# Performance work log

Measured on AMD Instinct MI355X. Metric: run time of the kernel, lower is better.

## Reference

```python
import jax, jax.numpy as jnp
import numpy as np

N = 100000
D = 128
E = 1600000
L = 3
LN_EPS = 1e-5
SM_EPS = 1e-16  # PyG softmax denominator eps
NEG_SLOPE = 0.2  # GATConv leaky_relu slope


def setup_inputs() -> dict:
    key = jax.random.key(0)
    ks = jax.random.split(key, 9)
    x = jax.random.normal(ks[0], (N, D), dtype=jnp.float32)
    edge_index = jax.random.randint(ks[1], (2, E), 0, N, dtype=jnp.int64)
    # Per-level GATConv params (heads=1, concat -> out dim D)
    W = jax.random.normal(ks[2], (L, D, D), dtype=jnp.float32) / np.sqrt(D)
    att_src = jax.random.normal(ks[3], (L, D), dtype=jnp.float32) / np.sqrt(D)
    att_dst = jax.random.normal(ks[4], (L, D), dtype=jnp.float32) / np.sqrt(D)
    bias = jnp.zeros((L, D), dtype=jnp.float32)
    ln_gamma = jnp.ones((L, D), dtype=jnp.float32)
    ln_beta = jnp.zeros((L, D), dtype=jnp.float32)
    return {"x": x, "edge_index": edge_index, "W": W, "att_src": att_src,
            "att_dst": att_dst, "bias": bias, "ln_gamma": ln_gamma, "ln_beta": ln_beta}


def _gat_level(x, src, dst, W, a_src, a_dst, b):
    h = x @ W                                   # [N, D] transformed features
    alpha_s = h @ a_src                         # [N] per-node src attention logit
    alpha_d = h @ a_dst                         # [N]
    alpha = alpha_s[src] + alpha_d[dst]         # [E'] edge logits
    alpha = jax.nn.leaky_relu(alpha, NEG_SLOPE)
    amax = jax.ops.segment_max(alpha, dst, num_segments=N)  # self-loops guarantee nonempty segments
    alpha = jnp.exp(alpha - amax[dst])
    denom = jax.ops.segment_sum(alpha, dst, num_segments=N)
    alpha = alpha / (denom[dst] + SM_EPS)       # segment softmax over incoming edges
    msg = h[src] * alpha[:, None]               # [E', D]
    out = jax.ops.segment_sum(msg, dst, num_segments=N)
    return out + b


def reference(x, edge_index, W, att_src, att_dst, bias, ln_gamma, ln_beta):
    loops = jnp.arange(N, dtype=edge_index.dtype)
    src = jnp.concatenate([edge_index[0], loops])  # PyG GATConv adds self-loops
    dst = jnp.concatenate([edge_index[1], loops])
    for i in range(L):
        x_att = _gat_level(x, src, dst, W[i], att_src[i], att_dst[i], bias[i])
        y = x + x_att
        mu = jnp.mean(y, axis=-1, keepdims=True)
        var = jnp.mean(jnp.square(y - mu), axis=-1, keepdims=True)
        y = (y - mu) * jax.lax.rsqrt(var + LN_EPS) * ln_gamma[i] + ln_beta[i]
        x = jax.nn.relu(y)  # dropout is identity in eval mode
    return x
```

## Files before the change

### kernel.cpp

```cpp
#include <hip/hip_runtime.h>
#include <hip/hip_fp16.h>
#include <cstdint>

#define D 128
#define NEG_SLOPE 0.2f
#define LN_EPS 1e-5f
#define SM_EPS 1e-16f


__global__ void hist_dst(const int* __restrict__ dst, int E, int* __restrict__ deg) {
    int e = blockIdx.x * blockDim.x + threadIdx.x;
    if (e < E) atomicAdd(&deg[dst[e]], 1);
}

__global__ void scanA(const int* __restrict__ deg, int n,
                      int* __restrict__ excl, int* __restrict__ bsums) {
    __shared__ int s[256];
    int t = threadIdx.x;
    int v = blockIdx.x * 256 + t;
    int d = (v < n) ? deg[v] : 0;
    s[t] = d;
    __syncthreads();
    for (int off = 1; off < 256; off <<= 1) {
        int tv = (t >= off) ? s[t - off] : 0;
        __syncthreads();
        s[t] += tv;
        __syncthreads();
    }
    if (v < n) excl[v] = s[t] - d;
    if (t == 255) bsums[blockIdx.x] = s[255];
}

__global__ void scanB(int* __restrict__ bsums, int nb) {
    __shared__ int s[512];
    int t = threadIdx.x;
    int v = (t < nb) ? bsums[t] : 0;
    s[t] = v;
    __syncthreads();
    for (int off = 1; off < 512; off <<= 1) {
        int tv = (t >= off) ? s[t - off] : 0;
        __syncthreads();
        s[t] += tv;
        __syncthreads();
    }
    if (t < nb) bsums[t] = s[t] - v;
}

__global__ void scanC(int* __restrict__ rowptr, const int* __restrict__ bsums,
                      int* __restrict__ cursor, int n, int total) {
    int v = blockIdx.x * blockDim.x + threadIdx.x;
    if (v < n) { rowptr[v] += bsums[v >> 8]; cursor[v] = 0; }
    if (v == 0) rowptr[n] = total;
}

__global__ void fill_csr(const int* __restrict__ src, const int* __restrict__ dst,
                         int E, const int* __restrict__ rowptr,
                         int* __restrict__ cursor, int* __restrict__ col) {
    int e = blockIdx.x * blockDim.x + threadIdx.x;
    if (e >= E) return;
    int d = dst[e];
    int p = rowptr[d] + atomicAdd(&cursor[d], 1);
    col[p] = src[e];
}


__global__ __launch_bounds__(256) void gemm_alpha(
        const float* __restrict__ x, const float* __restrict__ W,
        const float* __restrict__ asrc, const float* __restrict__ adst,
        __half* __restrict__ h, float* __restrict__ as_, float* __restrict__ ad_, int n) {
    __shared__ float sX[64][D];
    int t = threadIdx.x;
    int row0 = blockIdx.x * 64;

    const float4* xv = (const float4*)x;
    #pragma unroll
    for (int i = 0; i < 8; ++i) {
        int fid = i * 256 + t;
        int r = fid >> 5;
        int c4 = fid & 31;
        int gr = row0 + r;
        float4 val = (gr < n) ? xv[(size_t)gr * 32 + c4] : make_float4(0.f, 0.f, 0.f, 0.f);
        ((float4*)&sX[r][0])[c4] = val;
    }
    __syncthreads();

    int g = t >> 5, m = t & 31;
    int rbase = g * 8;
    float4 acc[8];
    #pragma unroll
    for (int r = 0; r < 8; ++r) acc[r] = make_float4(0.f, 0.f, 0.f, 0.f);

    const float4* Wv = (const float4*)W;
    #pragma unroll 4
    for (int k = 0; k < D; ++k) {
        float4 w = Wv[k * 32 + m];
        #pragma unroll
        for (int r = 0; r < 8; ++r) {
            float xval = sX[rbase + r][k];
            acc[r].x += xval * w.x;
            acc[r].y += xval * w.y;
            acc[r].z += xval * w.z;
            acc[r].w += xval * w.w;
        }
    }

    float4 a_s = ((const float4*)asrc)[m];
    float4 a_d = ((const float4*)adst)[m];
    #pragma unroll
    for (int r = 0; r < 8; ++r) {
        int gr = row0 + rbase + r;
        if (gr < n) {
            union { __half2 h2[2]; float2 f2; } u;
            u.h2[0] = __floats2half2_rn(acc[r].x, acc[r].y);
            u.h2[1] = __floats2half2_rn(acc[r].z, acc[r].w);
            ((float2*)(h + (size_t)gr * D))[m] = u.f2;
            float ps = acc[r].x * a_s.x + acc[r].y * a_s.y + acc[r].z * a_s.z + acc[r].w * a_s.w;
            float pd = acc[r].x * a_d.x + acc[r].y * a_d.y + acc[r].z * a_d.z + acc[r].w * a_d.w;
            #pragma unroll
            for (int d = 16; d >= 1; d >>= 1) {
                ps += __shfl_xor(ps, d);
                pd += __shfl_xor(pd, d);
            }
            if (m == 0) { as_[gr] = ps; ad_[gr] = pd; }
        }
    }
}


__global__ __launch_bounds__(256) void aggregate(
        const float* __restrict__ xin, const __half* __restrict__ h,
        const float* __restrict__ as_, const float* __restrict__ ad_,
        const int* __restrict__ col, const int* __restrict__ rowptr,
        const float* __restrict__ bias, const float* __restrict__ gamma,
        const float* __restrict__ beta, float* __restrict__ xout, int n) {
    __shared__ int   sS[4][64];
    __shared__ float sA[4][64];
    int tid = threadIdx.x;
    int wslot = tid >> 6;
    int lane = tid & 63;
    int wid = (int)((blockIdx.x * blockDim.x + tid) >> 6);
    if (wid >= n) return;
    int v = wid;
    int grp = lane >> 4;
    int gl  = lane & 15;
    int start = rowptr[v], end = rowptr[v + 1];
    float adv = ad_[v];
    float self_a = as_[v] + adv;
    self_a = (self_a > 0.f) ? self_a : NEG_SLOPE * self_a;

    float mval = self_a;
    for (int cb = start; cb < end; cb += 64) {
        int e = cb + lane;
        int   s_l = 0;
        float a_l = -1e30f;
        if (e < end) {
            s_l = col[e];
            float aa = as_[s_l] + adv;
            a_l = (aa > 0.f) ? aa : NEG_SLOPE * aa;
        }
        if (cb == start) { sS[wslot][lane] = s_l; sA[wslot][lane] = a_l; }
        mval = fmaxf(mval, a_l);
    }
    #pragma unroll
    for (int d = 32; d >= 1; d >>= 1) mval = fmaxf(mval, __shfl_xor(mval, d));

    float sacc = 0.f;
    float acc[8];
    #pragma unroll
    for (int j = 0; j < 8; ++j) acc[j] = 0.f;

    for (int cb = start; cb < end; cb += 64) {
        if (cb != start) {
            int e = cb + lane;
            int   s_l = 0;
            float a_l = -1e30f;
            if (e < end) {
                s_l = col[e];
                float aa = as_[s_l] + adv;
                a_l = (aa > 0.f) ? aa : NEG_SLOPE * aa;
            }
            sS[wslot][lane] = s_l; sA[wslot][lane] = a_l;
        }
        int cnt = min(64, end - cb);
        for (int i = grp; i < cnt; i += 4) {
            int s = sS[wslot][i];
            float w = __expf(sA[wslot][i] - mval);
            sacc += w;
            union { float4 f4; __half2 h2[4]; } u;
            u.f4 = ((const float4*)(h + (size_t)s * D))[gl];
            #pragma unroll
            for (int j = 0; j < 4; ++j) {
                float2 f = __half22float2(u.h2[j]);
                acc[2*j]   += w * f.x;
                acc[2*j+1] += w * f.y;
            }
        }
    }

    sacc += __shfl_xor(sacc, 16);
    sacc += __shfl_xor(sacc, 32);
    #pragma unroll
    for (int j = 0; j < 8; ++j) {
        acc[j] += __shfl_xor(acc[j], 16);
        acc[j] += __shfl_xor(acc[j], 32);
    }

    float w_self = __expf(self_a - mval);
    sacc += w_self;
    {
        union { float4 f4; __half2 h2[4]; } u;
        u.f4 = ((const float4*)(h + (size_t)v * D))[gl];
        #pragma unroll
        for (int j = 0; j < 4; ++j) {
            float2 f = __half22float2(u.h2[j]);
            acc[2*j]   += w_self * f.x;
            acc[2*j+1] += w_self * f.y;
        }
    }
    float inv = 1.f / (sacc + SM_EPS);

    const float4* xr = (const float4*)(xin + (size_t)v * D) + gl * 2;
    float4 xa = xr[0], xb = xr[1];
    const float4* b4 = (const float4*)bias  + gl * 2;
    float4 ba = b4[0], bb = b4[1];
    float y[8];
    y[0] = xa.x + acc[0] * inv + ba.x;
    y[1] = xa.y + acc[1] * inv + ba.y;
    y[2] = xa.z + acc[2] * inv + ba.z;
    y[3] = xa.w + acc[3] * inv + ba.w;
    y[4] = xb.x + acc[4] * inv + bb.x;
    y[5] = xb.y + acc[5] * inv + bb.y;
    y[6] = xb.z + acc[6] * inv + bb.z;
    y[7] = xb.w + acc[7] * inv + bb.w;

    float s2 = 0.f;
    #pragma unroll
    for (int j = 0; j < 8; ++j) s2 += y[j];
    #pragma unroll
    for (int d = 8; d >= 1; d >>= 1) s2 += __shfl_xor(s2, d);
    float mu = s2 * (1.f / 128.f);
    float vs = 0.f;
    #pragma unroll
    for (int j = 0; j < 8; ++j) { float dd = y[j] - mu; vs += dd * dd; }
    #pragma unroll
    for (int d = 8; d >= 1; d >>= 1) vs += __shfl_xor(vs, d);
    float rstd = rsqrtf(vs * (1.f / 128.f) + LN_EPS);

    const float4* g4 = (const float4*)gamma + gl * 2;
    const float4* t4 = (const float4*)beta  + gl * 2;
    float4 ga = g4[0], gb = g4[1];
    float4 ta = t4[0], tb = t4[1];
    float4 oa, ob;
    oa.x = fmaxf((y[0] - mu) * rstd * ga.x + ta.x, 0.f);
    oa.y = fmaxf((y[1] - mu) * rstd * ga.y + ta.y, 0.f);
    oa.z = fmaxf((y[2] - mu) * rstd * ga.z + ta.z, 0.f);
    oa.w = fmaxf((y[3] - mu) * rstd * ga.w + ta.w, 0.f);
    ob.x = fmaxf((y[4] - mu) * rstd * gb.x + tb.x, 0.f);
    ob.y = fmaxf((y[5] - mu) * rstd * gb.y + tb.y, 0.f);
    ob.z = fmaxf((y[6] - mu) * rstd * gb.z + tb.z, 0.f);
    ob.w = fmaxf((y[7] - mu) * rstd * gb.w + tb.w, 0.f);

    if (lane < 16) {
        float4* o4 = (float4*)(xout + (size_t)v * D) + gl * 2;
        o4[0] = oa;
        o4[1] = ob;
    }
}


extern "C" void kernel_launch(void* const* d_in, const int* in_sizes, int n_in,
                              void* d_out, int out_size, void* d_ws, size_t ws_size,
                              hipStream_t stream) {
    const float* x       = (const float*)d_in[0];
    const int*   edge    = (const int*)d_in[1];
    const float* W       = (const float*)d_in[2];
    const float* att_src = (const float*)d_in[3];
    const float* att_dst = (const float*)d_in[4];
    const float* bias    = (const float*)d_in[5];
    const float* gamma   = (const float*)d_in[6];
    const float* beta    = (const float*)d_in[7];
    float* out = (float*)d_out;

    const int N = in_sizes[0] / D;
    const int E = in_sizes[1] / 2;

    const int* src = edge;
    const int* dst = edge + E;

    char* ws = (char*)d_ws;
    size_t off = 0;
    auto carve = [&](size_t bytes) -> char* {
        char* p = ws + off;
        off = (off + bytes + 511) & ~(size_t)511;
        return p;
    };
    int*    rowptr = (int*)carve((size_t)(N + 1) * 4);
    int*    cursor = (int*)carve((size_t)N * 4);
    int*    bsums  = (int*)carve(512 * 4);
    int*    col    = (int*)carve((size_t)E * 4);
    __half* h      = (__half*)carve((size_t)N * D * 2);
    float*  as_    = (float*)carve((size_t)N * 4);
    float*  ad_    = (float*)carve((size_t)N * 4);
    float*  x1     = (float*)carve((size_t)N * D * 4);
    (void)ws_size;

    const int TPB = 256;
    int nbN  = (N + TPB - 1) / TPB;
    int nbE  = (E + TPB - 1) / TPB;

    hipMemsetAsync(cursor, 0, (size_t)N * 4, stream);
    hist_dst<<<nbE, TPB, 0, stream>>>(dst, E, cursor);
    scanA<<<nbN, TPB, 0, stream>>>(cursor, N, rowptr, bsums);
    scanB<<<1, 512, 0, stream>>>(bsums, nbN);
    scanC<<<nbN, TPB, 0, stream>>>(rowptr, bsums, cursor, N, E);
    fill_csr<<<nbE, TPB, 0, stream>>>(src, dst, E, rowptr, cursor, col);

    int gemmGrid = (N + 63) / 64;
    int aggGrid  = (N * 64 + TPB - 1) / TPB;

    const float* xin = x;
    float* bufs[3] = { x1, x1, out };
    for (int l = 0; l < 3; ++l) {
        const float* Wl  = W + (size_t)l * D * D;
        const float* asl = att_src + (size_t)l * D;
        const float* adl = att_dst + (size_t)l * D;
        const float* bl  = bias + (size_t)l * D;
        const float* gl  = gamma + (size_t)l * D;
        const float* btl = beta + (size_t)l * D;
        float* xout = bufs[l];

        gemm_alpha<<<gemmGrid, TPB, 0, stream>>>(xin, Wl, asl, adl, h, as_, ad_, N);
        aggregate<<<aggGrid, TPB, 0, stream>>>(xin, h, as_, ad_, col, rowptr,
                                               bl, gl, btl, xout, N);
        xin = xout;
    }
}
```

Measured before the change: 666.5 us.

## Use MFMA fp16 GEMM with folded attention vectors and half-precision aggregation

Replaces the FP32 scalar GEMM with an fp16 MFMA 16x16x32 kernel over 128-row tiles, staging x and a pre-transposed fp16 W in XOR-swizzled shared memory. A prep kernel folds att_src/att_dst into W (W·a), so the attention logits become dot products of x with precomputed vectors. The aggregation now computes exp weights once per edge instead of per group and accumulates messages with packed half2 FMAs. This cuts GEMM FP32 ALU cost and aggregation arithmetic, at the cost of lower precision: x is rounded to fp16 before the logits are computed, and the weighted sums accumulate in fp16, which risks overflow and accuracy loss.

```diff
diff --git a/kernel.cpp b/kernel.cpp
--- a/kernel.cpp
+++ b/kernel.cpp
@@ -6,6 +6,9 @@
 #define NEG_SLOPE 0.2f
 #define LN_EPS 1e-5f
 #define SM_EPS 1e-16f
+
+typedef _Float16 f16x8 __attribute__((ext_vector_type(8)));
+typedef float f32x4 __attribute__((ext_vector_type(4)));
 
 
 __global__ void hist_dst(const int* __restrict__ dst, int E, int* __restrict__ deg) {
@@ -64,66 +67,131 @@
 }
 
 
-__global__ __launch_bounds__(256) void gemm_alpha(
-        const float* __restrict__ x, const float* __restrict__ W,
-        const float* __restrict__ asrc, const float* __restrict__ adst,
+__global__ void prep_w(const float* __restrict__ W, const float* __restrict__ a_src,
+                       const float* __restrict__ a_dst, __half* __restrict__ Wt,
+                       float* __restrict__ wsv, float* __restrict__ wdv) {
+    int l = blockIdx.x;
+    const float* Wl = W + (size_t)l * D * D;
+    __half* Wtl = Wt + (size_t)l * D * D;
+    int t = threadIdx.x;
+    __shared__ float sA[D], sD[D];
+    if (t < D) { sA[t] = a_src[l * D + t]; sD[t] = a_dst[l * D + t]; }
+    __syncthreads();
+    if (t < D) {
+        float ps = 0.f, pd = 0.f;
+        for (int c = 0; c < D; ++c) {
+            float wv = Wl[t * D + c];
+            ps += wv * sA[c];
+            pd += wv * sD[c];
+        }
+        wsv[l * D + t] = ps;
+        wdv[l * D + t] = pd;
+    }
+    int c = t & 127, kh = t >> 7;
+    for (int g = 0; g < 8; ++g) {
+        int k0 = kh * 64 + g * 8;
+        union { __half hv[8]; float4 f4; } u;
+        #pragma unroll
+        for (int rr = 0; rr < 8; ++rr) u.hv[rr] = __float2half(Wl[(k0 + rr) * D + c]);
+        *(float4*)(Wtl + (size_t)c * D + k0) = u.f4;
+    }
+}
+
+
+__global__ __launch_bounds__(256) void gemm_mfma(
+        const float* __restrict__ x, const __half* __restrict__ Wt,
+        const float* __restrict__ wsv, const float* __restrict__ wdv,
         __half* __restrict__ h, float* __restrict__ as_, float* __restrict__ ad_, int n) {
-    __shared__ float sX[64][D];
+    __shared__ char sXa[32768];
+    __shared__ char sWb[32768];
     int t = threadIdx.x;
-    int row0 = blockIdx.x * 64;
+    int row0 = blockIdx.x * 128;
+    int lane = t & 63;
+    int w = t >> 6;
+    int wrow = (w >> 1) * 64;
+    int wcol = (w & 1) * 64;
 
     const float4* xv = (const float4*)x;
     #pragma unroll
+    for (int i = 0; i < 16; ++i) {
+        int slot = i * 256 + t;
+        int r = slot >> 5;
+        int c4 = slot & 31;
+        int gr = row0 + r;
+        float4 v = (gr < n) ? xv[(size_t)gr * 32 + c4] : make_float4(0.f, 0.f, 0.f, 0.f);
+        union { __half2 q[2]; float2 f; } u;
+        u.q[0] = __floats2half2_rn(v.x, v.y);
+        u.q[1] = __floats2half2_rn(v.z, v.w);
+        *(float2*)(sXa + r * 256 + ((c4 * 8) ^ ((r & 7) << 4))) = u.f;
+    }
+    const float4* wv = (const float4*)Wt;
+    #pragma unroll
     for (int i = 0; i < 8; ++i) {
-        int fid = i * 256 + t;
-        int r = fid >> 5;
-        int c4 = fid & 31;
-        int gr = row0 + r;
-        float4 val = (gr < n) ? xv[(size_t)gr * 32 + c4] : make_float4(0.f, 0.f, 0.f, 0.f);
-        ((float4*)&sX[r][0])[c4] = val;
+        int chunk = i * 256 + t;
+        int r = chunk >> 4;
+        int c16 = chunk & 15;
+        float4 v = wv[chunk];
+        *(float4*)(sWb + r * 256 + ((c16 * 16) ^ ((r & 7) << 4))) = v;
     }
     __syncthreads();
 
-    int g = t >> 5, m = t & 31;
-    int rbase = g * 8;
-    float4 acc[8];
-    #pragma unroll
-    for (int r = 0; r < 8; ++r) acc[r] = make_float4(0.f, 0.f, 0.f, 0.f);
-
-    const float4* Wv = (const float4*)W;
-    #pragma unroll 4
-    for (int k = 0; k < D; ++k) {
-        float4 w = Wv[k * 32 + m];
-        #pragma unroll
-        for (int r = 0; r < 8; ++r) {
-            float xval = sX[rbase + r][k];
-            acc[r].x += xval * w.x;
-            acc[r].y += xval * w.y;
-            acc[r].z += xval * w.z;
-            acc[r].w += xval * w.w;
-        }
-    }
-
-    float4 a_s = ((const float4*)asrc)[m];
-    float4 a_d = ((const float4*)adst)[m];
-    #pragma unroll
-    for (int r = 0; r < 8; ++r) {
-        int gr = row0 + rbase + r;
-        if (gr < n) {
-            union { __half2 h2[2]; float2 f2; } u;
-            u.h2[0] = __floats2half2_rn(acc[r].x, acc[r].y);
-            u.h2[1] = __floats2half2_rn(acc[r].z, acc[r].w);
-            ((float2*)(h + (size_t)gr * D))[m] = u.f2;
-            float ps = acc[r].x * a_s.x + acc[r].y * a_s.y + acc[r].z * a_s.z + acc[r].w * a_s.w;
-            float pd = acc[r].x * a_d.x + acc[r].y * a_d.y + acc[r].z * a_d.z + acc[r].w * a_d.w;
+    f32x4 acc[4][4];
+    #pragma unroll
+    for (int a = 0; a < 4; ++a)
+        #pragma unroll
+        for (int b = 0; b < 4; ++b) acc[a][b] = (f32x4){0.f, 0.f, 0.f, 0.f};
+
+    #pragma unroll
+    for (int ks = 0; ks < 4; ++ks) {
+        int kbyte = ks * 64 + (lane >> 4) * 16;
+        f16x8 aF[4], bF[4];
+        #pragma unroll
+        for (int tt = 0; tt < 4; ++tt) {
+            int ra = wrow + tt * 16 + (lane & 15);
+            aF[tt] = *(f16x8*)(sXa + ra * 256 + (kbyte ^ ((ra & 7) << 4)));
+            int rb = wcol + tt * 16 + (lane & 15);
+            bF[tt] = *(f16x8*)(sWb + rb * 256 + (kbyte ^ ((rb & 7) << 4)));
+        }
+        #pragma unroll
+        for (int tr = 0; tr < 4; ++tr)
             #pragma unroll
-            for (int d = 16; d >= 1; d >>= 1) {
-                ps += __shfl_xor(ps, d);
-                pd += __shfl_xor(pd, d);
+            for (int tc = 0; tc < 4; ++tc)
+                acc[tr][tc] = __builtin_amdgcn_mfma_f32_16x16x32_f16(aF[tr], bF[tc], acc[tr][tc], 0, 0, 0);
+    }
+
+    #pragma unroll
+    for (int tr = 0; tr < 4; ++tr) {
+        #pragma unroll
+        for (int reg = 0; reg < 4; ++reg) {
+            int gr = row0 + wrow + tr * 16 + (lane >> 4) * 4 + reg;
+            if (gr < n) {
+                #pragma unroll
+                for (int tc = 0; tc < 4; ++tc) {
+                    int gc = wcol + tc * 16 + (lane & 15);
+                    h[(size_t)gr * D + gc] = __float2half(acc[tr][tc][reg]);
+                }
             }
-            if (m == 0) { as_[gr] = ps; ad_[gr] = pd; }
-        }
-    }
+        }
+    }
+
+    int r = t >> 1, hh = t & 1;
+    float ps = 0.f, pd = 0.f;
+    const float4* s4 = (const float4*)wsv + hh * 16;
+    const float4* d4 = (const float4*)wdv + hh * 16;
+    #pragma unroll
+    for (int g = 0; g < 8; ++g) {
+        int kbyte = hh * 128 + g * 16;
+        f16x8 xa = *(f16x8*)(sXa + r * 256 + (kbyte ^ ((r & 7) << 4)));
+        float4 sa = s4[g * 2], sb = s4[g * 2 + 1];
+        float4 da = d4[g * 2], db = d4[g * 2 + 1];
+        ps += (float)xa[0] * sa.x + (float)xa[1] * sa.y + (float)xa[2] * sa.z + (float)xa[3] * sa.w
+            + (float)xa[4] * sb.x + (float)xa[5] * sb.y + (float)xa[6] * sb.z + (float)xa[7] * sb.w;
+        pd += (float)xa[0] * da.x + (float)xa[1] * da.y + (float)xa[2] * da.z + (float)xa[3] * da.w
+            + (float)xa[4] * db.x + (float)xa[5] * db.y + (float)xa[6] * db.z + (float)xa[7] * db.w;
+    }
+    ps += __shfl_xor(ps, 1);
+    pd += __shfl_xor(pd, 1);
+    if (hh == 0 && row0 + r < n) { as_[row0 + r] = ps; ad_[row0 + r] = pd; }
 }
 
 
@@ -133,8 +201,8 @@
         const int* __restrict__ col, const int* __restrict__ rowptr,
         const float* __restrict__ bias, const float* __restrict__ gamma,
         const float* __restrict__ beta, float* __restrict__ xout, int n) {
-    __shared__ int   sS[4][64];
-    __shared__ float sA[4][64];
+    __shared__ int     sS[4][64];
+    __shared__ __half2 sW[4][64];
     int tid = threadIdx.x;
     int wslot = tid >> 6;
     int lane = tid & 63;
@@ -149,56 +217,69 @@
     self_a = (self_a > 0.f) ? self_a : NEG_SLOPE * self_a;
 
     float mval = self_a;
+    int   s0 = 0;
+    float a0 = -1e30f;
     for (int cb = start; cb < end; cb += 64) {
         int e = cb + lane;
-        int   s_l = 0;
-        float a_l = -1e30f;
+        int   sl = 0;
+        float al = -1e30f;
         if (e < end) {
-            s_l = col[e];
-            float aa = as_[s_l] + adv;
-            a_l = (aa > 0.f) ? aa : NEG_SLOPE * aa;
-        }
-        if (cb == start) { sS[wslot][lane] = s_l; sA[wslot][lane] = a_l; }
-        mval = fmaxf(mval, a_l);
+            sl = col[e];
+            float aa = as_[sl] + adv;
+            al = (aa > 0.f) ? aa : NEG_SLOPE * aa;
+        }
+        if (cb == start) { s0 = sl; a0 = al; }
+        mval = fmaxf(mval, al);
     }
     #pragma unroll
     for (int d = 32; d >= 1; d >>= 1) mval = fmaxf(mval, __shfl_xor(mval, d));
 
-    float sacc = 0.f;
-    float acc[8];
-    #pragma unroll
-    for (int j = 0; j < 8; ++j) acc[j] = 0.f;
+    float wl = __expf(a0 - mval);
+    float sacc = wl;
+    sS[wslot][lane] = s0;
+    sW[wslot][lane] = __float2half2_rn(wl);
+
+    __half2 hacc[4];
+    #pragma unroll
+    for (int j = 0; j < 4; ++j) hacc[j] = __float2half2_rn(0.f);
+
+    const float4* h4 = (const float4*)h;
 
     for (int cb = start; cb < end; cb += 64) {
         if (cb != start) {
             int e = cb + lane;
-            int   s_l = 0;
-            float a_l = -1e30f;
+            int   sl = 0;
+            float al = -1e30f;
             if (e < end) {
-                s_l = col[e];
-                float aa = as_[s_l] + adv;
-                a_l = (aa > 0.f) ? aa : NEG_SLOPE * aa;
+                sl = col[e];
+                float aa = as_[sl] + adv;
+                al = (aa > 0.f) ? aa : NEG_SLOPE * aa;
             }
-            sS[wslot][lane] = s_l; sA[wslot][lane] = a_l;
+            float wl2 = __expf(al - mval);
+            sacc += wl2;
+            sS[wslot][lane] = sl;
+            sW[wslot][lane] = __float2half2_rn(wl2);
         }
         int cnt = min(64, end - cb);
         for (int i = grp; i < cnt; i += 4) {
             int s = sS[wslot][i];
-            float w = __expf(sA[wslot][i] - mval);
-            sacc += w;
+            __half2 w2 = sW[wslot][i];
             union { float4 f4; __half2 h2[4]; } u;
-            u.f4 = ((const float4*)(h + (size_t)s * D))[gl];
+            u.f4 = h4[(size_t)s * 16 + gl];
             #pragma unroll
-            for (int j = 0; j < 4; ++j) {
-                float2 f = __half22float2(u.h2[j]);
-                acc[2*j]   += w * f.x;
-                acc[2*j+1] += w * f.y;
-            }
-        }
-    }
-
-    sacc += __shfl_xor(sacc, 16);
-    sacc += __shfl_xor(sacc, 32);
+            for (int j = 0; j < 4; ++j) hacc[j] = __hfma2(u.h2[j], w2, hacc[j]);
+        }
+    }
+    #pragma unroll
+    for (int d = 32; d >= 1; d >>= 1) sacc += __shfl_xor(sacc, d);
+
+    float acc[8];
+    #pragma unroll
+    for (int j = 0; j < 4; ++j) {
+        float2 f = __half22float2(hacc[j]);
+        acc[2 * j] = f.x;
+        acc[2 * j + 1] = f.y;
+    }
     #pragma unroll
     for (int j = 0; j < 8; ++j) {
         acc[j] += __shfl_xor(acc[j], 16);
@@ -209,19 +290,19 @@
     sacc += w_self;
     {
         union { float4 f4; __half2 h2[4]; } u;
-        u.f4 = ((const float4*)(h + (size_t)v * D))[gl];
+        u.f4 = h4[(size_t)v * 16 + gl];
         #pragma unroll
         for (int j = 0; j < 4; ++j) {
             float2 f = __half22float2(u.h2[j]);
-            acc[2*j]   += w_self * f.x;
-            acc[2*j+1] += w_self * f.y;
+            acc[2 * j]     += w_self * f.x;
+            acc[2 * j + 1] += w_self * f.y;
         }
     }
     float inv = 1.f / (sacc + SM_EPS);
 
     const float4* xr = (const float4*)(xin + (size_t)v * D) + gl * 2;
     float4 xa = xr[0], xb = xr[1];
-    const float4* b4 = (const float4*)bias  + gl * 2;
+    const float4* b4 = (const float4*)bias + gl * 2;
     float4 ba = b4[0], bb = b4[1];
     float y[8];
     y[0] = xa.x + acc[0] * inv + ba.x;
@@ -247,7 +328,7 @@
     float rstd = rsqrtf(vs * (1.f / 128.f) + LN_EPS);
 
     const float4* g4 = (const float4*)gamma + gl * 2;
-    const float4* t4 = (const float4*)beta  + gl * 2;
+    const float4* t4 = (const float4*)beta + gl * 2;
     float4 ga = g4[0], gb = g4[1];
     float4 ta = t4[0], tb = t4[1];
     float4 oa, ob;
@@ -302,11 +383,16 @@
     float*  as_    = (float*)carve((size_t)N * 4);
     float*  ad_    = (float*)carve((size_t)N * 4);
     float*  x1     = (float*)carve((size_t)N * D * 4);
+    __half* Wt     = (__half*)carve((size_t)3 * D * D * 2);
+    float*  wsv    = (float*)carve((size_t)3 * D * 4);
+    float*  wdv    = (float*)carve((size_t)3 * D * 4);
     (void)ws_size;
 
     const int TPB = 256;
-    int nbN  = (N + TPB - 1) / TPB;
-    int nbE  = (E + TPB - 1) / TPB;
+    int nbN = (N + TPB - 1) / TPB;
+    int nbE = (E + TPB - 1) / TPB;
+
+    prep_w<<<3, TPB, 0, stream>>>(W, att_src, att_dst, Wt, wsv, wdv);
 
     hipMemsetAsync(cursor, 0, (size_t)N * 4, stream);
     hist_dst<<<nbE, TPB, 0, stream>>>(dst, E, cursor);
@@ -315,21 +401,21 @@
     scanC<<<nbN, TPB, 0, stream>>>(rowptr, bsums, cursor, N, E);
     fill_csr<<<nbE, TPB, 0, stream>>>(src, dst, E, rowptr, cursor, col);
 
-    int gemmGrid = (N + 63) / 64;
+    int gemmGrid = (N + 127) / 128;
     int aggGrid  = (N * 64 + TPB - 1) / TPB;
 
     const float* xin = x;
     float* bufs[3] = { x1, x1, out };
     for (int l = 0; l < 3; ++l) {
-        const float* Wl  = W + (size_t)l * D * D;
-        const float* asl = att_src + (size_t)l * D;
-        const float* adl = att_dst + (size_t)l * D;
-        const float* bl  = bias + (size_t)l * D;
-        const float* gl  = gamma + (size_t)l * D;
-        const float* btl = beta + (size_t)l * D;
+        const __half* Wtl = Wt + (size_t)l * D * D;
+        const float*  wsl = wsv + (size_t)l * D;
+        const float*  wdl = wdv + (size_t)l * D;
+        const float*  bl  = bias + (size_t)l * D;
+        const float*  gl  = gamma + (size_t)l * D;
+        const float*  btl = beta + (size_t)l * D;
         float* xout = bufs[l];
 
-        gemm_alpha<<<gemmGrid, TPB, 0, stream>>>(xin, Wl, asl, adl, h, as_, ad_, N);
+        gemm_mfma<<<gemmGrid, TPB, 0, stream>>>(xin, Wtl, wsl, wdl, h, as_, ad_, N);
         aggregate<<<aggGrid, TPB, 0, stream>>>(xin, h, as_, ad_, col, rowptr,
                                                bl, gl, btl, xout, N);
         xin = xout;
```

Measured after the change: 626.3 us. -6.0%, faster.
